# Performance work log

Hardware: AMD Instinct MI355X
Metric: run time of the kernel (lower is better)

## Reference

```python
import jax, jax.numpy as jnp
import numpy as np

EPS = 1e-4

def setup_inputs() -> dict:
    key = jax.random.key(0)
    x = jax.random.normal(key, (16, 256, 8192), dtype=jnp.float32)
    return {"x": x}

def reference(x):
    # x: [B, C, T]; cumulative (causal) normalization along time axis
    T = x.shape[-1]
    count = jnp.arange(1, T + 1, dtype=x.dtype).reshape(1, 1, T)
    cum_sum = jnp.cumsum(x, axis=-1)
    cum_pow_sum = jnp.cumsum(x * x, axis=-1)
    cum_mean = cum_sum / count
    cum_var = cum_pow_sum / count - cum_mean * cum_mean
    cum_std = jnp.sqrt(cum_var + EPS)
    return (x - cum_mean) / cum_std
```

## Files before the change

kernel.cpp:

```cpp
#include <hip/hip_runtime.h>

#define ROW_T   8192
#define THREADS 256
#define WPB     4
#define NT      32
#define PIPE    8
#define EPSV    1e-4f

typedef float fvec4 __attribute__((ext_vector_type(4)));

template<int CTRL, int RM>
__device__ __forceinline__ float dpp_add(float v) {
    const int p = __builtin_amdgcn_update_dpp(0, __float_as_int(v), CTRL, RM, 0xf, true);
    return v + __int_as_float(p);
}

__device__ __forceinline__ float wave_incl_scan(float v) {
    v = dpp_add<0x111, 0xf>(v);
    v = dpp_add<0x112, 0xf>(v);
    v = dpp_add<0x114, 0xf>(v);
    v = dpp_add<0x118, 0xf>(v);
    v = dpp_add<0x142, 0xa>(v);
    v = dpp_add<0x143, 0xc>(v);
    return v;
}

__global__ __launch_bounds__(THREADS, 4)
void cumnorm_kernel(const float* __restrict__ x, float* __restrict__ out) {
    const int lane = threadIdx.x & 63;
    const int wid  = threadIdx.x >> 6;

    const long long row = (long long)blockIdx.x * WPB + wid;
    const float* __restrict__ xr   = x   + row * ROW_T;
    float* __restrict__       outr = out + row * ROW_T;
    const int l4 = lane * 4;

    fvec4 B[PIPE];
    #pragma unroll
    for (int k = 0; k < PIPE; ++k)
        B[k] = *reinterpret_cast<const fvec4*>(xr + k * 256 + l4);

    float carry_s = 0.f, carry_ss = 0.f;

    #pragma unroll
    for (int k = 0; k < NT; ++k) {
        const fvec4 c = B[k & (PIPE - 1)];
        if (k + PIPE < NT)
            B[k & (PIPE - 1)] = *reinterpret_cast<const fvec4*>(xr + (k + PIPE) * 256 + l4);

        float s  = (c.x + c.y) + (c.z + c.w);
        float ss = fmaf(c.x, c.x, fmaf(c.y, c.y, fmaf(c.z, c.z, c.w * c.w)));

        const float is  = wave_incl_scan(s);
        const float iss = wave_incl_scan(ss);

        float S  = carry_s  + (is  - s);
        float SS = carry_ss + (iss - ss);

        carry_s  += __int_as_float(__builtin_amdgcn_readlane(__float_as_int(is),  63));
        carry_ss += __int_as_float(__builtin_amdgcn_readlane(__float_as_int(iss), 63));

        const int e0 = k * 256 + l4;
        fvec4 o;
#define CN_STEP(v, idx, dst) {                                            \
        S += (v); SS = fmaf((v), (v), SS);                                \
        const float inv  = __builtin_amdgcn_rcpf((float)(e0 + (idx) + 1));\
        const float mean = S * inv;                                       \
        const float var  = fmaf(SS, inv, -(mean * mean));                 \
        (dst) = ((v) - mean) * __builtin_amdgcn_rsqf(var + EPSV);         \
    }
        CN_STEP(c.x, 0, o.x)
        CN_STEP(c.y, 1, o.y)
        CN_STEP(c.z, 2, o.z)
        CN_STEP(c.w, 3, o.w)
#undef CN_STEP

        *reinterpret_cast<fvec4*>(outr + e0) = o;
    }
}

extern "C" void kernel_launch(void* const* d_in, const int* in_sizes, int n_in,
                              void* d_out, int out_size, void* d_ws, size_t ws_size,
                              hipStream_t stream) {
    const float* x = (const float*)d_in[0];
    float* out = (float*)d_out;
    const int rows = out_size / ROW_T;
    cumnorm_kernel<<<rows / WPB, THREADS, 0, stream>>>(x, out);
}
```

Baseline: 232.9 us.

## Deepen load pipeline and issue loads and stores via inline asm with exact vmcnt waits

Raises the prefetch depth from 8 to 12 tiles. Loads and stores become inline-asm global_load/global_store instructions inside a recursively unrolled template. Each tile waits with an exact s_waitcnt vmcnt count, so only its own load is awaited, not every outstanding memory op. With only one wave per SIMD, this targets memory latency that the compiler's conservative waits left exposed. The risk is that the compiler sees the asm outputs as ready at once, so correctness relies on the manual waits and sched barriers, and the extra buffers raise register pressure.

```diff
diff --git a/kernel.cpp b/kernel.cpp
--- a/kernel.cpp
+++ b/kernel.cpp
@@ -4,7 +4,7 @@
 #define THREADS 256
 #define WPB     4
 #define NT      32
-#define PIPE    8
+#define PIPE    12
 #define EPSV    1e-4f
 
 typedef float fvec4 __attribute__((ext_vector_type(4)));
@@ -14,7 +14,6 @@
     const int p = __builtin_amdgcn_update_dpp(0, __float_as_int(v), CTRL, RM, 0xf, true);
     return v + __int_as_float(p);
 }
-
 __device__ __forceinline__ float wave_incl_scan(float v) {
     v = dpp_add<0x111, 0xf>(v);
     v = dpp_add<0x112, 0xf>(v);
@@ -25,43 +24,44 @@
     return v;
 }
 
-__global__ __launch_bounds__(THREADS, 4)
-void cumnorm_kernel(const float* __restrict__ x, float* __restrict__ out) {
-    const int lane = threadIdx.x & 63;
-    const int wid  = threadIdx.x >> 6;
+template<int K>
+__device__ __forceinline__ void prologue(const float* __restrict__ pa, fvec4 (&B)[PIPE]) {
+    asm volatile("global_load_dwordx4 %0, %1, off" : "=v"(B[K]) : "v"(pa + K * 256));
+    if constexpr (K + 1 < PIPE) prologue<K + 1>(pa, B);
+}
 
-    const long long row = (long long)blockIdx.x * WPB + wid;
-    const float* __restrict__ xr   = x   + row * ROW_T;
-    float* __restrict__       outr = out + row * ROW_T;
-    const int l4 = lane * 4;
+template<int K>
+__device__ __forceinline__ void tile(const float* __restrict__ pa,
+                                     float* __restrict__ po,
+                                     fvec4 (&B)[PIPE],
+                                     float& carry_s, float& carry_ss, const int l4) {
+    constexpr int LOADS_AFTER  = (PIPE - 1) < (NT - 1 - K) ? (PIPE - 1) : (NT - 1 - K);
+    constexpr int STORES_AFTER = (PIPE < K) ? PIPE : K;
+    constexpr int N = LOADS_AFTER + STORES_AFTER;
 
-    fvec4 B[PIPE];
-    #pragma unroll
-    for (int k = 0; k < PIPE; ++k)
-        B[k] = *reinterpret_cast<const fvec4*>(xr + k * 256 + l4);
+    asm volatile("s_waitcnt vmcnt(%0)" :: "i"(N));
+    __builtin_amdgcn_sched_barrier(0);
 
-    float carry_s = 0.f, carry_ss = 0.f;
+    const fvec4 c = B[K % PIPE];
 
-    #pragma unroll
-    for (int k = 0; k < NT; ++k) {
-        const fvec4 c = B[k & (PIPE - 1)];
-        if (k + PIPE < NT)
-            B[k & (PIPE - 1)] = *reinterpret_cast<const fvec4*>(xr + (k + PIPE) * 256 + l4);
+    if constexpr (K + PIPE < NT)
+        asm volatile("global_load_dwordx4 %0, %1, off"
+                     : "=v"(B[K % PIPE]) : "v"(pa + (K + PIPE) * 256));
 
-        float s  = (c.x + c.y) + (c.z + c.w);
-        float ss = fmaf(c.x, c.x, fmaf(c.y, c.y, fmaf(c.z, c.z, c.w * c.w)));
+    float s  = (c.x + c.y) + (c.z + c.w);
+    float ss = fmaf(c.x, c.x, fmaf(c.y, c.y, fmaf(c.z, c.z, c.w * c.w)));
 
-        const float is  = wave_incl_scan(s);
-        const float iss = wave_incl_scan(ss);
+    const float is  = wave_incl_scan(s);
+    const float iss = wave_incl_scan(ss);
 
-        float S  = carry_s  + (is  - s);
-        float SS = carry_ss + (iss - ss);
+    float S  = carry_s  + (is  - s);
+    float SS = carry_ss + (iss - ss);
 
-        carry_s  += __int_as_float(__builtin_amdgcn_readlane(__float_as_int(is),  63));
-        carry_ss += __int_as_float(__builtin_amdgcn_readlane(__float_as_int(iss), 63));
+    carry_s  += __int_as_float(__builtin_amdgcn_readlane(__float_as_int(is),  63));
+    carry_ss += __int_as_float(__builtin_amdgcn_readlane(__float_as_int(iss), 63));
 
-        const int e0 = k * 256 + l4;
-        fvec4 o;
+    const int e0 = K * 256 + l4;
+    fvec4 o;
 #define CN_STEP(v, idx, dst) {                                            \
         S += (v); SS = fmaf((v), (v), SS);                                \
         const float inv  = __builtin_amdgcn_rcpf((float)(e0 + (idx) + 1));\
@@ -69,14 +69,34 @@
         const float var  = fmaf(SS, inv, -(mean * mean));                 \
         (dst) = ((v) - mean) * __builtin_amdgcn_rsqf(var + EPSV);         \
     }
-        CN_STEP(c.x, 0, o.x)
-        CN_STEP(c.y, 1, o.y)
-        CN_STEP(c.z, 2, o.z)
-        CN_STEP(c.w, 3, o.w)
+    CN_STEP(c.x, 0, o.x)
+    CN_STEP(c.y, 1, o.y)
+    CN_STEP(c.z, 2, o.z)
+    CN_STEP(c.w, 3, o.w)
 #undef CN_STEP
 
-        *reinterpret_cast<fvec4*>(outr + e0) = o;
-    }
+    asm volatile("global_store_dwordx4 %0, %1, off" :: "v"(po + K * 256), "v"(o));
+
+    if constexpr (K + 1 < NT) tile<K + 1>(pa, po, B, carry_s, carry_ss, l4);
+}
+
+__global__ __launch_bounds__(THREADS, 4)
+void cumnorm_kernel(const float* __restrict__ x, float* __restrict__ out) {
+    const int lane = threadIdx.x & 63;
+    const int wid  = threadIdx.x >> 6;
+
+    const long long row = (long long)blockIdx.x * WPB + wid;
+    const int l4 = lane * 4;
+    const float* __restrict__ pa = x   + row * ROW_T + l4;
+    float* __restrict__       po = out + row * ROW_T + l4;
+
+    fvec4 B[PIPE];
+    prologue<0>(pa, B);
+
+    float carry_s = 0.f, carry_ss = 0.f;
+    tile<0>(pa, po, B, carry_s, carry_ss, l4);
+
+    asm volatile("s_waitcnt vmcnt(0)");
 }
 
 extern "C" void kernel_launch(void* const* d_in, const int* in_sizes, int n_in,
```

Result: no change. 232.2 us (-0.3%).

## Split per-row scan into chunk-sum and normalize kernels for full parallelism

Applied to the files above, without the earlier changes.

Replaces the single-wave-per-row serial scan with two kernels. The first computes per-256-element chunk sums and sums of squares into workspace. The second scans those chunk totals per row and normalizes each chunk independently. This targets the low occupancy and long serial dependency chain of the row loop, at the cost of reading the input twice and adding a second launch.

```diff
diff --git a/kernel.cpp b/kernel.cpp
--- a/kernel.cpp
+++ b/kernel.cpp
@@ -1,21 +1,21 @@
 #include <hip/hip_runtime.h>
 
 #define ROW_T   8192
+#define CHUNK   256
+#define CPR     (ROW_T / CHUNK)
 #define THREADS 256
 #define WPB     4
-#define NT      32
-#define PIPE    8
 #define EPSV    1e-4f
 
 typedef float fvec4 __attribute__((ext_vector_type(4)));
+typedef float fvec2 __attribute__((ext_vector_type(2)));
 
 template<int CTRL, int RM>
 __device__ __forceinline__ float dpp_add(float v) {
     const int p = __builtin_amdgcn_update_dpp(0, __float_as_int(v), CTRL, RM, 0xf, true);
     return v + __int_as_float(p);
 }
-
-__device__ __forceinline__ float wave_incl_scan(float v) {
+__device__ __forceinline__ float scan64(float v) {
     v = dpp_add<0x111, 0xf>(v);
     v = dpp_add<0x112, 0xf>(v);
     v = dpp_add<0x114, 0xf>(v);
@@ -24,44 +24,59 @@
     v = dpp_add<0x143, 0xc>(v);
     return v;
 }
+__device__ __forceinline__ float scan32(float v) {
+    v = dpp_add<0x111, 0xf>(v);
+    v = dpp_add<0x112, 0xf>(v);
+    v = dpp_add<0x114, 0xf>(v);
+    v = dpp_add<0x118, 0xf>(v);
+    v = dpp_add<0x142, 0xa>(v);
+    return v;
+}
 
-__global__ __launch_bounds__(THREADS, 4)
-void cumnorm_kernel(const float* __restrict__ x, float* __restrict__ out) {
+__global__ __launch_bounds__(THREADS, 8)
+void sums_kernel(const float* __restrict__ x, fvec2* __restrict__ ws) {
     const int lane = threadIdx.x & 63;
     const int wid  = threadIdx.x >> 6;
+    const long long g = (long long)blockIdx.x * WPB + wid;
 
-    const long long row = (long long)blockIdx.x * WPB + wid;
-    const float* __restrict__ xr   = x   + row * ROW_T;
-    float* __restrict__       outr = out + row * ROW_T;
-    const int l4 = lane * 4;
+    const fvec4 c = *reinterpret_cast<const fvec4*>(x + g * CHUNK + lane * 4);
+    float s  = (c.x + c.y) + (c.z + c.w);
+    float ss = fmaf(c.x, c.x, fmaf(c.y, c.y, fmaf(c.z, c.z, c.w * c.w)));
+    const float ts  = scan64(s);
+    const float tss = scan64(ss);
+    if (lane == 63) ws[g] = fvec2{ts, tss};
+}
 
-    fvec4 B[PIPE];
-    #pragma unroll
-    for (int k = 0; k < PIPE; ++k)
-        B[k] = *reinterpret_cast<const fvec4*>(xr + k * 256 + l4);
+__global__ __launch_bounds__(THREADS, 8)
+void norm_kernel(const float* __restrict__ x, const fvec2* __restrict__ ws,
+                 float* __restrict__ out) {
+    const int lane = threadIdx.x & 63;
+    const int wid  = threadIdx.x >> 6;
+    const long long g = (long long)blockIdx.x * WPB + wid;
+    const int cidx = (int)(g & (CPR - 1));
+    const long long rowc0 = g - cidx;
 
-    float carry_s = 0.f, carry_ss = 0.f;
+    const fvec4 c = *reinterpret_cast<const fvec4*>(x + g * CHUNK + lane * 4);
 
-    #pragma unroll
-    for (int k = 0; k < NT; ++k) {
-        const fvec4 c = B[k & (PIPE - 1)];
-        if (k + PIPE < NT)
-            B[k & (PIPE - 1)] = *reinterpret_cast<const fvec4*>(xr + (k + PIPE) * 256 + l4);
+    const fvec2 t = ws[rowc0 + (lane & 31)];
+    const float ps  = scan32(t.x);
+    const float pss = scan32(t.y);
+    float S0 = 0.f, SS0 = 0.f;
+    if (cidx > 0) {
+        S0  = __int_as_float(__builtin_amdgcn_readlane(__float_as_int(ps),  cidx - 1));
+        SS0 = __int_as_float(__builtin_amdgcn_readlane(__float_as_int(pss), cidx - 1));
+    }
 
-        float s  = (c.x + c.y) + (c.z + c.w);
-        float ss = fmaf(c.x, c.x, fmaf(c.y, c.y, fmaf(c.z, c.z, c.w * c.w)));
+    float s  = (c.x + c.y) + (c.z + c.w);
+    float ss = fmaf(c.x, c.x, fmaf(c.y, c.y, fmaf(c.z, c.z, c.w * c.w)));
+    const float is  = scan64(s);
+    const float iss = scan64(ss);
 
-        const float is  = wave_incl_scan(s);
-        const float iss = wave_incl_scan(ss);
+    float S  = S0  + (is  - s);
+    float SS = SS0 + (iss - ss);
 
-        float S  = carry_s  + (is  - s);
-        float SS = carry_ss + (iss - ss);
-
-        carry_s  += __int_as_float(__builtin_amdgcn_readlane(__float_as_int(is),  63));
-        carry_ss += __int_as_float(__builtin_amdgcn_readlane(__float_as_int(iss), 63));
-
-        const int e0 = k * 256 + l4;
-        fvec4 o;
+    const int e0 = cidx * CHUNK + lane * 4;
+    fvec4 o;
 #define CN_STEP(v, idx, dst) {                                            \
         S += (v); SS = fmaf((v), (v), SS);                                \
         const float inv  = __builtin_amdgcn_rcpf((float)(e0 + (idx) + 1));\
@@ -69,14 +84,13 @@
         const float var  = fmaf(SS, inv, -(mean * mean));                 \
         (dst) = ((v) - mean) * __builtin_amdgcn_rsqf(var + EPSV);         \
     }
-        CN_STEP(c.x, 0, o.x)
-        CN_STEP(c.y, 1, o.y)
-        CN_STEP(c.z, 2, o.z)
-        CN_STEP(c.w, 3, o.w)
+    CN_STEP(c.x, 0, o.x)
+    CN_STEP(c.y, 1, o.y)
+    CN_STEP(c.z, 2, o.z)
+    CN_STEP(c.w, 3, o.w)
 #undef CN_STEP
 
-        *reinterpret_cast<fvec4*>(outr + e0) = o;
-    }
+    *reinterpret_cast<fvec4*>(out + g * CHUNK + lane * 4) = o;
 }
 
 extern "C" void kernel_launch(void* const* d_in, const int* in_sizes, int n_in,
@@ -84,6 +98,10 @@
                               hipStream_t stream) {
     const float* x = (const float*)d_in[0];
     float* out = (float*)d_out;
-    const int rows = out_size / ROW_T;
-    cumnorm_kernel<<<rows / WPB, THREADS, 0, stream>>>(x, out);
+    fvec2* ws = (fvec2*)d_ws;
+    const int rows   = out_size / ROW_T;
+    const int blocks = rows * CPR / WPB;
+
+    sums_kernel<<<blocks, THREADS, 0, stream>>>(x, ws);
+    norm_kernel<<<blocks, THREADS, 0, stream>>>(x, ws, out);
 }
```

After: 239.8 us. 1.03x slower.
